# Kernel tuning notes

Measured on AMD Instinct MI355X. Metric: run time of the kernel, lower is better.

## Reference

```python
import jax, jax.numpy as jnp
import numpy as np

N, E = 50000, 800000
IN_CH, OUT_CH, MSG_DIM, TIME_DIM = 128, 128, 128, 128
HEADS = 2
HEAD_C = OUT_CH // HEADS  # 64
EDGE_DIM = MSG_DIM + TIME_DIM  # 256


def setup_inputs() -> dict:
    key = jax.random.key(0)
    ks = jax.random.split(key, 16)
    s = 0.05
    return {
        "x": jax.random.normal(ks[0], (N, IN_CH), jnp.float32),
        "last_update": jax.random.uniform(ks[1], (N,), jnp.float32),
        "t": jax.random.uniform(ks[2], (E,), jnp.float32),
        "msg": jax.random.normal(ks[3], (E, MSG_DIM), jnp.float32),
        "edge_index": jax.random.randint(ks[4], (2, E), 0, N, jnp.int64),
        # TimeEncoder: Linear(1, TIME_DIM) then cos
        "W_time": jax.random.normal(ks[5], (1, TIME_DIM), jnp.float32) * s,
        "b_time": jax.random.normal(ks[6], (TIME_DIM,), jnp.float32) * s,
        # TransformerConv linears (stored [in, out])
        "Wq": jax.random.normal(ks[7], (IN_CH, OUT_CH), jnp.float32) * s,
        "bq": jax.random.normal(ks[8], (OUT_CH,), jnp.float32) * s,
        "Wk": jax.random.normal(ks[9], (IN_CH, OUT_CH), jnp.float32) * s,
        "bk": jax.random.normal(ks[10], (OUT_CH,), jnp.float32) * s,
        "Wv": jax.random.normal(ks[11], (IN_CH, OUT_CH), jnp.float32) * s,
        "bv": jax.random.normal(ks[12], (OUT_CH,), jnp.float32) * s,
        "We": jax.random.normal(ks[13], (EDGE_DIM, OUT_CH), jnp.float32) * s,  # lin_edge, no bias
        "Ws": jax.random.normal(ks[14], (IN_CH, OUT_CH), jnp.float32) * s,  # lin_skip (root weight)
        "bs": jax.random.normal(ks[15], (OUT_CH,), jnp.float32) * s,
    }


def reference(x, last_update, t, msg, edge_index, W_time, b_time,
              Wq, bq, Wk, bk, Wv, bv, We, Ws, bs):
    src, dst = edge_index[0], edge_index[1]
    # --- temporal edge features ---
    rel_t = last_update[src] - t                      # [E]
    rel_t_enc = jnp.cos(rel_t[:, None] * W_time[0] + b_time)  # [E, TIME_DIM]
    edge_attr = jnp.concatenate([rel_t_enc, msg], axis=-1)    # [E, EDGE_DIM]
    # --- TransformerConv (heads=2, concat=True, root_weight=True, eval: no dropout) ---
    q = (x @ Wq + bq).reshape(N, HEADS, HEAD_C)[dst]   # [E,H,C] query at destination
    k = (x @ Wk + bk).reshape(N, HEADS, HEAD_C)[src]   # [E,H,C] key at source
    v = (x @ Wv + bv).reshape(N, HEADS, HEAD_C)[src]   # [E,H,C]
    e = (edge_attr @ We).reshape(E, HEADS, HEAD_C)     # [E,H,C]
    k = k + e
    alpha = jnp.sum(q * k, axis=-1) / jnp.sqrt(jnp.asarray(HEAD_C, x.dtype))  # [E,H]
    # segment softmax over edges grouped by destination node
    m = jax.ops.segment_max(alpha, dst, num_segments=N)       # [N,H]
    p = jnp.exp(alpha - m[dst])                               # [E,H]
    denom = jax.ops.segment_sum(p, dst, num_segments=N)       # [N,H]
    attn = p / denom[dst]                                     # [E,H]
    out_e = attn[:, :, None] * (v + e)                        # [E,H,C]
    out = jax.ops.segment_sum(out_e, dst, num_segments=N).reshape(N, HEADS * HEAD_C)
    return out + x @ Ws + bs
```

## Files before the change

### kernel.cpp

```cpp
#include <hip/hip_runtime.h>
#include <math.h>

#define N_NODES 50000
#define N_EDGES 800000
#define CH 128
#define GDIM 512

__global__ __launch_bounds__(256) void build_M_kernel(
    const float* __restrict__ Wq, const float* __restrict__ We,
    float* __restrict__ M)
{
    __shared__ float wq[CH];
    const int i = blockIdx.x, t = threadIdx.x;
    if (t < CH) wq[t] = Wq[i * CH + t];
    __syncthreads();
    #pragma unroll
    for (int rep = 0; rep < 2; ++rep) {
        int f  = rep * 256 + t;
        int h  = f >> 8, jj = f & 255;
        const float* wer = We + (size_t)jj * CH + h * 64;
        const float* wqr = wq + h * 64;
        float s = 0.f;
        #pragma unroll 8
        for (int c = 0; c < 64; ++c) s = fmaf(wqr[c], wer[c], s);
        M[(size_t)i * GDIM + f] = s;
    }
}

__global__ void build_gbias_kernel(const float* __restrict__ bq,
                                   const float* __restrict__ We,
                                   float* __restrict__ gb)
{
    int f = blockIdx.x * 256 + threadIdx.x;
    int h = f >> 8, jj = f & 255;
    float s = 0.f;
    #pragma unroll 8
    for (int c = 0; c < 64; ++c)
        s = fmaf(bq[h * 64 + c], We[(size_t)jj * CH + h * 64 + c], s);
    gb[f] = s;
}

__global__ __launch_bounds__(256) void node_linear_kernel(
    const float* __restrict__ x,
    const float* __restrict__ Wq, const float* __restrict__ bq,
    const float* __restrict__ Wk, const float* __restrict__ bk,
    const float* __restrict__ Wv, const float* __restrict__ bv,
    const float* __restrict__ Ws, const float* __restrict__ bs,
    const float* __restrict__ M,  const float* __restrict__ gb,
    float* __restrict__ Q, float* __restrict__ K,
    float* __restrict__ V, float* __restrict__ S, float* __restrict__ G)
{
    __shared__ float xs[64][CH];
    const int t  = threadIdx.x;
    const int n0 = blockIdx.x * 64;

    #pragma unroll
    for (int r = 0; r < 8; ++r) {
        int flat4 = r * 256 + t;
        int row   = flat4 >> 5;
        int c4    = (flat4 & 31) * 4;
        int gr    = n0 + row; if (gr >= N_NODES) gr = N_NODES - 1;
        *(float4*)&xs[row][c4] = *(const float4*)&x[(size_t)gr * CH + c4];
    }
    __syncthreads();

    const int tx = t & 31, ey = t >> 5;
    const int c0 = tx * 4, e0 = ey * 8;

    const float* Wp[8]   = {Wq, Wk, Wv, Ws, M, M + 128, M + 256, M + 384};
    const int    wstr[8] = {CH, CH, CH, CH, GDIM, GDIM, GDIM, GDIM};
    const float* Bp[8]   = {bq, bk, bv, bs, gb, gb + 128, gb + 256, gb + 384};
    float*       Op[8]   = {Q, K, V, S, G, G + 128, G + 256, G + 384};
    const int    ostr[8] = {CH, CH, CH, CH, GDIM, GDIM, GDIM, GDIM};

    #pragma unroll
    for (int m = 0; m < 8; ++m) {
        const float* W = Wp[m];
        const int ws_ = wstr[m];
        float4 acc[8];
        #pragma unroll
        for (int i = 0; i < 8; ++i) acc[i] = make_float4(0.f, 0.f, 0.f, 0.f);
        for (int j = 0; j < CH; ++j) {
            float4 w = *(const float4*)&W[(size_t)j * ws_ + c0];
            #pragma unroll
            for (int i = 0; i < 8; ++i) {
                float a = xs[e0 + i][j];
                acc[i].x = fmaf(a, w.x, acc[i].x);
                acc[i].y = fmaf(a, w.y, acc[i].y);
                acc[i].z = fmaf(a, w.z, acc[i].z);
                acc[i].w = fmaf(a, w.w, acc[i].w);
            }
        }
        float4 b4 = *(const float4*)&Bp[m][c0];
        float* O  = Op[m];
        const int os = ostr[m];
        #pragma unroll
        for (int i = 0; i < 8; ++i) {
            int n = n0 + e0 + i;
            if (n < N_NODES) {
                float4 r = make_float4(acc[i].x + b4.x, acc[i].y + b4.y,
                                       acc[i].z + b4.z, acc[i].w + b4.w);
                *(float4*)&O[(size_t)n * os + c0] = r;
            }
        }
    }
}

__global__ void hist_kernel(const int* __restrict__ ei, int* __restrict__ cnt)
{
    int e = blockIdx.x * 256 + threadIdx.x;
    atomicAdd(&cnt[ei[N_EDGES + e]], 1);
}

__global__ __launch_bounds__(1024) void scan_kernel(
    const int* __restrict__ cnt, int* __restrict__ base, int* __restrict__ cursor)
{
    __shared__ int ssum[1024];
    const int t = threadIdx.x;
    const int STRIP = 49;
    const int s0 = t * STRIP;
    int sum = 0;
    for (int i = 0; i < STRIP; ++i) {
        int idx = s0 + i;
        sum += (idx < N_NODES) ? cnt[idx] : 0;
    }
    ssum[t] = sum;
    __syncthreads();
    for (int off = 1; off < 1024; off <<= 1) {
        int v = (t >= off) ? ssum[t - off] : 0;
        __syncthreads();
        ssum[t] += v;
        __syncthreads();
    }
    int run = (t > 0) ? ssum[t - 1] : 0;
    for (int i = 0; i < STRIP; ++i) {
        int idx = s0 + i;
        if (idx < N_NODES) {
            base[idx] = run; cursor[idx] = run;
            run += cnt[idx];
        }
    }
    if (t == 1023) base[N_NODES] = ssum[1023];
}

__global__ void scatter_kernel(const int* __restrict__ ei, int* __restrict__ cursor,
                               int* __restrict__ ssrc, int* __restrict__ seid)
{
    int e = blockIdx.x * 256 + threadIdx.x;
    int d = ei[N_EDGES + e];
    int pos = atomicAdd(&cursor[d], 1);
    ssrc[pos] = ei[e];
    seid[pos] = e;
}

__global__ __launch_bounds__(256) void gather_attn_kernel(
    const float* __restrict__ last_update,
    const float* __restrict__ t_arr,
    const float* __restrict__ msg,
    const float* __restrict__ W_time,
    const float* __restrict__ b_time,
    const float* __restrict__ We,
    const float* __restrict__ Q, const float* __restrict__ K,
    const float* __restrict__ V, const float* __restrict__ S,
    const float* __restrict__ G,
    const int* __restrict__ base, const int* __restrict__ ssrc,
    const int* __restrict__ seid,
    float* __restrict__ out)
{
    __shared__ float wabuf[4][GDIM];
    const int wv = threadIdx.x >> 6;
    const int j  = threadIdx.x & 63;
    const int n  = blockIdx.x * 4 + wv;

    const float q0 = Q[(size_t)n * CH + j];
    const float q1 = Q[(size_t)n * CH + 64 + j];
    const float* gn = G + (size_t)n * GDIM + j;
    const float g00 = gn[0],   g01 = gn[64],  g02 = gn[128], g03 = gn[192];
    const float g10 = gn[256], g11 = gn[320], g12 = gn[384], g13 = gn[448];
    const float wt0 = W_time[j], wt1 = W_time[64 + j];
    const float bt0 = b_time[j], bt1 = b_time[64 + j];

    float wa00 = 0.f, wa01 = 0.f, wa02 = 0.f, wa03 = 0.f;
    float wa10 = 0.f, wa11 = 0.f, wa12 = 0.f, wa13 = 0.f;
    float nv0 = 0.f, nv1 = 0.f, den0 = 0.f, den1 = 0.f;

    const int b0 = base[n], b1 = base[n + 1];
    for (int i = b0; i < b1; ++i) {
        int src = ssrc[i];
        int eid = seid[i];
        float rt  = last_update[src] - t_arr[eid];
        float ea0 = __cosf(fmaf(rt, wt0, bt0));
        float ea1 = __cosf(fmaf(rt, wt1, bt1));
        float ea2 = msg[(size_t)eid * CH + j];
        float ea3 = msg[(size_t)eid * CH + 64 + j];
        float k0  = K[(size_t)src * CH + j];
        float k1  = K[(size_t)src * CH + 64 + j];
        float v0  = V[(size_t)src * CH + j];
        float v1  = V[(size_t)src * CH + 64 + j];

        float p0 = q0 * k0 + ea0 * g00 + ea1 * g01 + ea2 * g02 + ea3 * g03;
        float p1 = q1 * k1 + ea0 * g10 + ea1 * g11 + ea2 * g12 + ea3 * g13;
        p0 += __shfl_xor(p0, 1);  p1 += __shfl_xor(p1, 1);
        p0 += __shfl_xor(p0, 2);  p1 += __shfl_xor(p1, 2);
        p0 += __shfl_xor(p0, 4);  p1 += __shfl_xor(p1, 4);
        p0 += __shfl_xor(p0, 8);  p1 += __shfl_xor(p1, 8);
        p0 += __shfl_xor(p0, 16); p1 += __shfl_xor(p1, 16);
        p0 += __shfl_xor(p0, 32); p1 += __shfl_xor(p1, 32);
        p0 = __expf(p0 * 0.125f);
        p1 = __expf(p1 * 0.125f);

        den0 += p0; den1 += p1;
        wa00 = fmaf(p0, ea0, wa00); wa01 = fmaf(p0, ea1, wa01);
        wa02 = fmaf(p0, ea2, wa02); wa03 = fmaf(p0, ea3, wa03);
        wa10 = fmaf(p1, ea0, wa10); wa11 = fmaf(p1, ea1, wa11);
        wa12 = fmaf(p1, ea2, wa12); wa13 = fmaf(p1, ea3, wa13);
        nv0  = fmaf(p0, v0, nv0);
        nv1  = fmaf(p1, v1, nv1);
    }

    wabuf[wv][j]       = wa00; wabuf[wv][64 + j]  = wa01;
    wabuf[wv][128 + j] = wa02; wabuf[wv][192 + j] = wa03;
    wabuf[wv][256 + j] = wa10; wabuf[wv][320 + j] = wa11;
    wabuf[wv][384 + j] = wa12; wabuf[wv][448 + j] = wa13;
    __syncthreads();

    float a0 = 0.f, a1 = 0.f;
    #pragma unroll 4
    for (int jj = 0; jj < 256; ++jj) {
        float w0 = wabuf[wv][jj];
        float w1 = wabuf[wv][256 + jj];
        a0 = fmaf(w0, We[(size_t)jj * CH + j], a0);
        a1 = fmaf(w1, We[(size_t)jj * CH + 64 + j], a1);
    }

    float r0 = (b1 > b0) ? (nv0 + a0) / den0 : 0.f;
    float r1 = (b1 > b0) ? (nv1 + a1) / den1 : 0.f;
    out[(size_t)n * CH + j]      = r0 + S[(size_t)n * CH + j];
    out[(size_t)n * CH + 64 + j] = r1 + S[(size_t)n * CH + 64 + j];
}

extern "C" void kernel_launch(void* const* d_in, const int* in_sizes, int n_in,
                              void* d_out, int out_size, void* d_ws, size_t ws_size,
                              hipStream_t stream) {
    const float* x           = (const float*)d_in[0];
    const float* last_update = (const float*)d_in[1];
    const float* t           = (const float*)d_in[2];
    const float* msg         = (const float*)d_in[3];
    const int*   edge_index  = (const int*)d_in[4];
    const float* W_time      = (const float*)d_in[5];
    const float* b_time      = (const float*)d_in[6];
    const float* Wq = (const float*)d_in[7];
    const float* bq = (const float*)d_in[8];
    const float* Wk = (const float*)d_in[9];
    const float* bk = (const float*)d_in[10];
    const float* Wv = (const float*)d_in[11];
    const float* bv = (const float*)d_in[12];
    const float* We = (const float*)d_in[13];
    const float* Ws = (const float*)d_in[14];
    const float* bs = (const float*)d_in[15];
    float* out = (float*)d_out;

    float* ws = (float*)d_ws;
    const size_t NC = (size_t)N_NODES * CH;
    float* Q  = ws;
    float* K  = Q + NC;
    float* V  = K + NC;
    float* S  = V + NC;
    float* G  = S + NC;
    float* M  = G + (size_t)N_NODES * GDIM;
    float* gb = M + (size_t)CH * GDIM;
    int* cnt    = (int*)(gb + GDIM);
    int* base   = cnt + N_NODES;
    int* cursor = base + N_NODES + 1;
    int* ssrc   = cursor + N_NODES;
    int* seid   = ssrc + N_EDGES;

    hipMemsetAsync(cnt, 0, (size_t)N_NODES * sizeof(int), stream);

    build_M_kernel<<<CH, 256, 0, stream>>>(Wq, We, M);
    build_gbias_kernel<<<2, 256, 0, stream>>>(bq, We, gb);

    node_linear_kernel<<<(N_NODES + 63) / 64, 256, 0, stream>>>(
        x, Wq, bq, Wk, bk, Wv, bv, Ws, bs, M, gb, Q, K, V, S, G);

    hist_kernel<<<N_EDGES / 256, 256, 0, stream>>>(edge_index, cnt);
    scan_kernel<<<1, 1024, 0, stream>>>(cnt, base, cursor);
    scatter_kernel<<<N_EDGES / 256, 256, 0, stream>>>(edge_index, cursor, ssrc, seid);

    gather_attn_kernel<<<N_NODES / 4, 256, 0, stream>>>(
        last_update, t, msg, W_time, b_time, We,
        Q, K, V, S, G, base, ssrc, seid, out);
}
```

Before: 1.287 ms.

## Precompute rel_t in scatter, unroll gather loop by two, DPP reductions, share We loads

The scatter kernel now writes packed (src, eid) pairs and the precomputed relative time, so the gather kernel no longer does the dependent last_update/t lookups. The per-node edge loop is unrolled by two to keep more independent gathers in flight, and the wave reductions use DPP/swizzle instead of shuffles. The epilogue matvec against We is reorganised so each thread handles one column for two nodes, so every We load is reused across two nodes. This adds an extra srt array write and read and more register pressure in the unrolled loop.

```diff
diff --git a/kernel.cpp b/kernel.cpp
--- a/kernel.cpp
+++ b/kernel.cpp
@@ -143,19 +143,36 @@
     if (t == 1023) base[N_NODES] = ssum[1023];
 }
 
-__global__ void scatter_kernel(const int* __restrict__ ei, int* __restrict__ cursor,
-                               int* __restrict__ ssrc, int* __restrict__ seid)
+__global__ void scatter_kernel(const int* __restrict__ ei,
+                               const float* __restrict__ last_update,
+                               const float* __restrict__ t_arr,
+                               int* __restrict__ cursor,
+                               int2* __restrict__ sedge,
+                               float* __restrict__ srt)
 {
     int e = blockIdx.x * 256 + threadIdx.x;
+    int s = ei[e];
     int d = ei[N_EDGES + e];
     int pos = atomicAdd(&cursor[d], 1);
-    ssrc[pos] = ei[e];
-    seid[pos] = e;
+    sedge[pos] = make_int2(s, e);
+    srt[pos] = last_update[s] - t_arr[e];
+}
+
+__device__ __forceinline__ float wave_allsum(float p) {
+    p += __int_as_float(__builtin_amdgcn_update_dpp(
+            0, __float_as_int(p), 0xB1, 0xF, 0xF, true));
+    p += __int_as_float(__builtin_amdgcn_update_dpp(
+            0, __float_as_int(p), 0x4E, 0xF, 0xF, true));
+    p += __int_as_float(__builtin_amdgcn_update_dpp(
+            0, __float_as_int(p), 0x141, 0xF, 0xF, true));
+    p += __int_as_float(__builtin_amdgcn_update_dpp(
+            0, __float_as_int(p), 0x140, 0xF, 0xF, true));
+    p += __int_as_float(__builtin_amdgcn_ds_swizzle(__float_as_int(p), 0x401F));
+    p += __shfl_xor(p, 32);
+    return p;
 }
 
 __global__ __launch_bounds__(256) void gather_attn_kernel(
-    const float* __restrict__ last_update,
-    const float* __restrict__ t_arr,
     const float* __restrict__ msg,
     const float* __restrict__ W_time,
     const float* __restrict__ b_time,
@@ -163,11 +180,15 @@
     const float* __restrict__ Q, const float* __restrict__ K,
     const float* __restrict__ V, const float* __restrict__ S,
     const float* __restrict__ G,
-    const int* __restrict__ base, const int* __restrict__ ssrc,
-    const int* __restrict__ seid,
+    const int* __restrict__ base,
+    const int2* __restrict__ sedge,
+    const float* __restrict__ srt,
     float* __restrict__ out)
 {
     __shared__ float wabuf[4][GDIM];
+    __shared__ float nvbuf[4][CH];
+    __shared__ float dsh[4][2];
+    __shared__ int   degsh[4];
     const int wv = threadIdx.x >> 6;
     const int j  = threadIdx.x & 63;
     const int n  = blockIdx.x * 4 + wv;
@@ -185,27 +206,77 @@
     float nv0 = 0.f, nv1 = 0.f, den0 = 0.f, den1 = 0.f;
 
     const int b0 = base[n], b1 = base[n + 1];
-    for (int i = b0; i < b1; ++i) {
-        int src = ssrc[i];
-        int eid = seid[i];
-        float rt  = last_update[src] - t_arr[eid];
+    int i = b0;
+
+    for (; i + 2 <= b1; i += 2) {
+        const int2  seA = sedge[i];
+        const int2  seB = sedge[i + 1];
+        const float rtA = srt[i];
+        const float rtB = srt[i + 1];
+        const float* mA  = msg + (size_t)seA.y * CH;
+        const float* mB  = msg + (size_t)seB.y * CH;
+        const float* kpA = K   + (size_t)seA.x * CH;
+        const float* kpB = K   + (size_t)seB.x * CH;
+        const float* vpA = V   + (size_t)seA.x * CH;
+        const float* vpB = V   + (size_t)seB.x * CH;
+
+        float ea2A = mA[j],      ea3A = mA[64 + j];
+        float ea2B = mB[j],      ea3B = mB[64 + j];
+        float k0A  = kpA[j],     k1A  = kpA[64 + j];
+        float k0B  = kpB[j],     k1B  = kpB[64 + j];
+        float v0A  = vpA[j],     v1A  = vpA[64 + j];
+        float v0B  = vpB[j],     v1B  = vpB[64 + j];
+
+        float ea0A = __cosf(fmaf(rtA, wt0, bt0));
+        float ea1A = __cosf(fmaf(rtA, wt1, bt1));
+        float ea0B = __cosf(fmaf(rtB, wt0, bt0));
+        float ea1B = __cosf(fmaf(rtB, wt1, bt1));
+
+        float pA0 = fmaf(q0, k0A, fmaf(ea0A, g00, fmaf(ea1A, g01, fmaf(ea2A, g02, ea3A * g03))));
+        float pA1 = fmaf(q1, k1A, fmaf(ea0A, g10, fmaf(ea1A, g11, fmaf(ea2A, g12, ea3A * g13))));
+        float pB0 = fmaf(q0, k0B, fmaf(ea0B, g00, fmaf(ea1B, g01, fmaf(ea2B, g02, ea3B * g03))));
+        float pB1 = fmaf(q1, k1B, fmaf(ea0B, g10, fmaf(ea1B, g11, fmaf(ea2B, g12, ea3B * g13))));
+
+        pA0 = wave_allsum(pA0);
+        pA1 = wave_allsum(pA1);
+        pB0 = wave_allsum(pB0);
+        pB1 = wave_allsum(pB1);
+
+        pA0 = __expf(pA0 * 0.125f);
+        pA1 = __expf(pA1 * 0.125f);
+        pB0 = __expf(pB0 * 0.125f);
+        pB1 = __expf(pB1 * 0.125f);
+
+        den0 += pA0; den0 += pB0;
+        den1 += pA1; den1 += pB1;
+        wa00 = fmaf(pA0, ea0A, wa00); wa00 = fmaf(pB0, ea0B, wa00);
+        wa01 = fmaf(pA0, ea1A, wa01); wa01 = fmaf(pB0, ea1B, wa01);
+        wa02 = fmaf(pA0, ea2A, wa02); wa02 = fmaf(pB0, ea2B, wa02);
+        wa03 = fmaf(pA0, ea3A, wa03); wa03 = fmaf(pB0, ea3B, wa03);
+        wa10 = fmaf(pA1, ea0A, wa10); wa10 = fmaf(pB1, ea0B, wa10);
+        wa11 = fmaf(pA1, ea1A, wa11); wa11 = fmaf(pB1, ea1B, wa11);
+        wa12 = fmaf(pA1, ea2A, wa12); wa12 = fmaf(pB1, ea2B, wa12);
+        wa13 = fmaf(pA1, ea3A, wa13); wa13 = fmaf(pB1, ea3B, wa13);
+        nv0  = fmaf(pA0, v0A, nv0);   nv0  = fmaf(pB0, v0B, nv0);
+        nv1  = fmaf(pA1, v1A, nv1);   nv1  = fmaf(pB1, v1B, nv1);
+    }
+
+    if (i < b1) {
+        const int2  se = sedge[i];
+        const float rt = srt[i];
+        const float* m  = msg + (size_t)se.y * CH;
+        const float* kp = K   + (size_t)se.x * CH;
+        const float* vp = V   + (size_t)se.x * CH;
+        float ea2 = m[j],  ea3 = m[64 + j];
+        float k0  = kp[j], k1  = kp[64 + j];
+        float v0  = vp[j], v1  = vp[64 + j];
         float ea0 = __cosf(fmaf(rt, wt0, bt0));
         float ea1 = __cosf(fmaf(rt, wt1, bt1));
-        float ea2 = msg[(size_t)eid * CH + j];
-        float ea3 = msg[(size_t)eid * CH + 64 + j];
-        float k0  = K[(size_t)src * CH + j];
-        float k1  = K[(size_t)src * CH + 64 + j];
-        float v0  = V[(size_t)src * CH + j];
-        float v1  = V[(size_t)src * CH + 64 + j];
-
-        float p0 = q0 * k0 + ea0 * g00 + ea1 * g01 + ea2 * g02 + ea3 * g03;
-        float p1 = q1 * k1 + ea0 * g10 + ea1 * g11 + ea2 * g12 + ea3 * g13;
-        p0 += __shfl_xor(p0, 1);  p1 += __shfl_xor(p1, 1);
-        p0 += __shfl_xor(p0, 2);  p1 += __shfl_xor(p1, 2);
-        p0 += __shfl_xor(p0, 4);  p1 += __shfl_xor(p1, 4);
-        p0 += __shfl_xor(p0, 8);  p1 += __shfl_xor(p1, 8);
-        p0 += __shfl_xor(p0, 16); p1 += __shfl_xor(p1, 16);
-        p0 += __shfl_xor(p0, 32); p1 += __shfl_xor(p1, 32);
+
+        float p0 = fmaf(q0, k0, fmaf(ea0, g00, fmaf(ea1, g01, fmaf(ea2, g02, ea3 * g03))));
+        float p1 = fmaf(q1, k1, fmaf(ea0, g10, fmaf(ea1, g11, fmaf(ea2, g12, ea3 * g13))));
+        p0 = wave_allsum(p0);
+        p1 = wave_allsum(p1);
         p0 = __expf(p0 * 0.125f);
         p1 = __expf(p1 * 0.125f);
 
@@ -222,21 +293,38 @@
     wabuf[wv][128 + j] = wa02; wabuf[wv][192 + j] = wa03;
     wabuf[wv][256 + j] = wa10; wabuf[wv][320 + j] = wa11;
     wabuf[wv][384 + j] = wa12; wabuf[wv][448 + j] = wa13;
+    nvbuf[wv][j]      = nv0;
+    nvbuf[wv][64 + j] = nv1;
+    if (j == 0) {
+        dsh[wv][0] = den0; dsh[wv][1] = den1;
+        degsh[wv]  = b1 - b0;
+    }
     __syncthreads();
 
-    float a0 = 0.f, a1 = 0.f;
-    #pragma unroll 4
+    const int col = threadIdx.x & 127;
+    const int pr  = threadIdx.x >> 7;
+    const int h   = col >> 6;
+    const int nA  = 2 * pr, nB = 2 * pr + 1;
+    const int wo  = h * 256;
+
+    float aA = 0.f, aB = 0.f;
+    #pragma unroll 8
     for (int jj = 0; jj < 256; ++jj) {
-        float w0 = wabuf[wv][jj];
-        float w1 = wabuf[wv][256 + jj];
-        a0 = fmaf(w0, We[(size_t)jj * CH + j], a0);
-        a1 = fmaf(w1, We[(size_t)jj * CH + 64 + j], a1);
-    }
-
-    float r0 = (b1 > b0) ? (nv0 + a0) / den0 : 0.f;
-    float r1 = (b1 > b0) ? (nv1 + a1) / den1 : 0.f;
-    out[(size_t)n * CH + j]      = r0 + S[(size_t)n * CH + j];
-    out[(size_t)n * CH + 64 + j] = r1 + S[(size_t)n * CH + 64 + j];
+        float w = We[(size_t)jj * CH + col];
+        aA = fmaf(wabuf[nA][wo + jj], w, aA);
+        aB = fmaf(wabuf[nB][wo + jj], w, aB);
+    }
+
+    {
+        int node = blockIdx.x * 4 + nA;
+        float r = (degsh[nA] > 0) ? (nvbuf[nA][col] + aA) / dsh[nA][h] : 0.f;
+        out[(size_t)node * CH + col] = r + S[(size_t)node * CH + col];
+    }
+    {
+        int node = blockIdx.x * 4 + nB;
+        float r = (degsh[nB] > 0) ? (nvbuf[nB][col] + aB) / dsh[nB][h] : 0.f;
+        out[(size_t)node * CH + col] = r + S[(size_t)node * CH + col];
+    }
 }
 
 extern "C" void kernel_launch(void* const* d_in, const int* in_sizes, int n_in,
@@ -272,8 +360,10 @@
     int* cnt    = (int*)(gb + GDIM);
     int* base   = cnt + N_NODES;
     int* cursor = base + N_NODES + 1;
-    int* ssrc   = cursor + N_NODES;
-    int* seid   = ssrc + N_EDGES;
+    size_t off = (size_t)((char*)(cursor + N_NODES) - (char*)d_ws);
+    off = (off + 7) & ~(size_t)7;
+    int2*  sedge = (int2*)((char*)d_ws + off);
+    float* srt   = (float*)(sedge + N_EDGES);
 
     hipMemsetAsync(cnt, 0, (size_t)N_NODES * sizeof(int), stream);
 
@@ -285,9 +375,10 @@
 
     hist_kernel<<<N_EDGES / 256, 256, 0, stream>>>(edge_index, cnt);
     scan_kernel<<<1, 1024, 0, stream>>>(cnt, base, cursor);
-    scatter_kernel<<<N_EDGES / 256, 256, 0, stream>>>(edge_index, cursor, ssrc, seid);
+    scatter_kernel<<<N_EDGES / 256, 256, 0, stream>>>(
+        edge_index, last_update, t, cursor, sedge, srt);
 
     gather_attn_kernel<<<N_NODES / 4, 256, 0, stream>>>(
-        last_update, t, msg, W_time, b_time, We,
-        Q, K, V, S, G, base, ssrc, seid, out);
-}
+        msg, W_time, b_time, We,
+        Q, K, V, S, G, base, sedge, srt, out);
+}
```

Measured after the change: 1.167 ms. -9.3%, faster.
